# Kernel optimization log

Hardware: AMD Instinct MI355X
Metric: run time of the kernel (lower is better)

## Reference

```python
import jax, jax.numpy as jnp
import numpy as np

Q_MAX = 127.0  # 2**(8-1) - 1
EPS = 1e-08


def quantize_activation(x):
    # per-tensor symmetric int8 quant with STE
    scale = jnp.maximum(jnp.max(jnp.abs(x)) / Q_MAX, EPS)
    x_scaled = x / scale
    rounded = jnp.clip(jnp.round(x_scaled), -Q_MAX, Q_MAX)
    # STE: forward = rounded, backward = identity w.r.t. x_scaled
    q = x_scaled + jax.lax.stop_gradient(rounded - x_scaled)
    return q, jax.lax.stop_gradient(scale)


def ternarize_weight(W):
    scale = jnp.mean(jnp.abs(W)) + EPS
    W_norm = W / scale
    rounded = jnp.clip(jnp.round(W_norm), -1.0, 1.0)
    # STE: forward = rounded, backward = identity w.r.t. W
    tW = W + jax.lax.stop_gradient(rounded - W)
    return tW, jax.lax.stop_gradient(scale)


def setup_inputs() -> dict:
    key = jax.random.key(0)
    kx, kw = jax.random.split(key)
    in_features, out_features = 4096, 11008
    x = jax.random.normal(kx, (4, 2048, in_features), dtype=jnp.float32)
    # kaiming_uniform_(a=sqrt(5)) -> U(-bound, bound), bound = sqrt(6/((1+a^2)*fan_in)) = 1/sqrt(fan_in)
    bound = 1.0 / np.sqrt(in_features)
    W = jax.random.uniform(kw, (out_features, in_features), dtype=jnp.float32,
                           minval=-bound, maxval=bound)
    return {"x": x, "W": W}


def reference(x, W):
    qx, act_scale = quantize_activation(x)
    tW, w_scale = ternarize_weight(W)
    # F.linear: x @ W.T ; [b, s, in] x [out, in] -> [b, s, out]
    out = jnp.einsum('bsi,oi->bso', qx, tW)
    return out * (w_scale * act_scale)
```

## Files before the change

### kernel.cpp

```cpp
#include <hip/hip_runtime.h>
#include <cstdint>

typedef int i32x4 __attribute__((ext_vector_type(4)));
typedef int i32x16 __attribute__((ext_vector_type(16)));

#define M_DIM 8192
#define N_DIM 11008
#define K_DIM 4096
#define NT    (K_DIM / 128)

#define WS_AMAX_OFF   0
#define WS_WSUM_OFF   4096
#define WS_SCALES_OFF 12288
#define WS_QX_OFF     16384
#define WS_TW_OFF     (16384 + 33554432)

__device__ __forceinline__ void gload_lds16(const void* g, void* l) {
  __builtin_amdgcn_global_load_lds(
      (const __attribute__((address_space(1))) unsigned int*)g,
      (__attribute__((address_space(3))) unsigned int*)l, 16, 0, 0);
}


__global__ void reduce_amax(const float* __restrict__ x, float* __restrict__ partial, int n4) {
  const float4* xv = (const float4*)x;
  float m = 0.f;
  for (long i = (long)blockIdx.x * blockDim.x + threadIdx.x; i < n4;
       i += (long)gridDim.x * blockDim.x) {
    float4 v = xv[i];
    m = fmaxf(m, fmaxf(fmaxf(fabsf(v.x), fabsf(v.y)), fmaxf(fabsf(v.z), fabsf(v.w))));
  }
  __shared__ float sm[256];
  sm[threadIdx.x] = m;
  __syncthreads();
  for (int s = 128; s > 0; s >>= 1) {
    if (threadIdx.x < s) sm[threadIdx.x] = fmaxf(sm[threadIdx.x], sm[threadIdx.x + s]);
    __syncthreads();
  }
  if (threadIdx.x == 0) partial[blockIdx.x] = sm[0];
}

__global__ void reduce_wsum(const float* __restrict__ w, double* __restrict__ partial, int n4) {
  const float4* wv = (const float4*)w;
  double acc = 0.0;
  for (long i = (long)blockIdx.x * blockDim.x + threadIdx.x; i < n4;
       i += (long)gridDim.x * blockDim.x) {
    float4 v = wv[i];
    acc += (double)fabsf(v.x) + (double)fabsf(v.y) + (double)fabsf(v.z) + (double)fabsf(v.w);
  }
  __shared__ double sd[256];
  sd[threadIdx.x] = acc;
  __syncthreads();
  for (int s = 128; s > 0; s >>= 1) {
    if (threadIdx.x < s) sd[threadIdx.x] += sd[threadIdx.x + s];
    __syncthreads();
  }
  if (threadIdx.x == 0) partial[blockIdx.x] = sd[0];
}

__global__ void finalize_scales(const float* __restrict__ amax_p,
                                const double* __restrict__ wsum_p,
                                float* __restrict__ scales) {
  __shared__ float sm[1024];
  __shared__ double sd[1024];
  const int t = threadIdx.x;
  sm[t] = amax_p[t];
  sd[t] = wsum_p[t];
  __syncthreads();
  for (int s = 512; s > 0; s >>= 1) {
    if (t < s) {
      sm[t] = fmaxf(sm[t], sm[t + s]);
      sd[t] += sd[t + s];
    }
    __syncthreads();
  }
  if (t == 0) {
    float act_scale = fmaxf(sm[0] / 127.0f, 1e-8f);
    float w_scale = (float)(sd[0] / (double)((long long)N_DIM * K_DIM)) + 1e-8f;
    scales[0] = act_scale;
    scales[1] = w_scale;
    scales[2] = act_scale * w_scale;
  }
}


__device__ __forceinline__ int quant_clip(float v, float s, float lim) {
  float r = rintf(v / s);
  r = fminf(fmaxf(r, -lim), lim);
  return (int)r;
}

__global__ void quant_x(const float* __restrict__ x, const float* __restrict__ scales,
                        int8_t* __restrict__ q) {
  const float s = scales[0];
  const long i = (long)blockIdx.x * blockDim.x + threadIdx.x;
  const float4* xv = (const float4*)x + (i << 2);
  i32x4 pk;
#pragma unroll
  for (int j = 0; j < 4; ++j) {
    float4 v = xv[j];
    int b0 = quant_clip(v.x, s, 127.f);
    int b1 = quant_clip(v.y, s, 127.f);
    int b2 = quant_clip(v.z, s, 127.f);
    int b3 = quant_clip(v.w, s, 127.f);
    pk[j] = (b0 & 255) | ((b1 & 255) << 8) | ((b2 & 255) << 16) | (b3 << 24);
  }
  *((i32x4*)q + i) = pk;
}

__global__ void tern_w(const float* __restrict__ w, const float* __restrict__ scales,
                       int8_t* __restrict__ q) {
  const float s = scales[1];
  const long i = (long)blockIdx.x * blockDim.x + threadIdx.x;
  const float4* wv = (const float4*)w + (i << 2);
  i32x4 pk;
#pragma unroll
  for (int j = 0; j < 4; ++j) {
    float4 v = wv[j];
    int b0 = quant_clip(v.x, s, 1.f);
    int b1 = quant_clip(v.y, s, 1.f);
    int b2 = quant_clip(v.z, s, 1.f);
    int b3 = quant_clip(v.w, s, 1.f);
    pk[j] = (b0 & 255) | ((b1 & 255) << 8) | ((b2 & 255) << 16) | (b3 << 24);
  }
  *((i32x4*)q + i) = pk;
}


__global__ __launch_bounds__(512, 2) void gemm_i8(const int8_t* __restrict__ qx,
                                                  const int8_t* __restrict__ tw,
                                                  const float* __restrict__ scales,
                                                  float* __restrict__ out) {
  __shared__ __align__(16) int8_t lds[4][32768];

  const int tid = threadIdx.x;
  const int l = tid & 63;
  const int w = tid >> 6;

  const int bid = blockIdx.x;
  const int xcd = bid & 7;
  const int local = bid >> 3;
  const int ni = local >> 2;
  const int mi = (xcd << 2) + (local & 3);
  const long row0 = (long)mi << 8;
  const long col0 = (long)ni << 8;

  const int srow = tid >> 3;
  const int sch = (tid & 7) ^ (srow & 7);
  const int8_t* pA = qx + (row0 + srow) * (long)K_DIM + (sch << 4);
  const int8_t* pB = tw + (col0 + srow) * (long)K_DIM + (sch << 4);
  const int ldst = w << 10;

  auto stage_part = [&](int8_t* dA, int8_t* dB, int kt, int part) {
    const long cb = (long)kt << 7;
    gload_lds16(pA + cb + ((long)part * 64) * K_DIM, dA + part * 8192 + ldst);
    gload_lds16(pB + cb + ((long)part * 64) * K_DIM, dB + part * 8192 + ldst);
  };

  const int lane31 = l & 31;
  const int khalf = l >> 5;
  const int swz = l & 7;
  int cOff[4];
#pragma unroll
  for (int ks = 0; ks < 4; ++ks) cOff[ks] = ((((ks << 1) | khalf) ^ swz) << 4);
  const int aRow = ((w >> 2) * 128 + lane31) * 128;
  const int bRow0 = ((w & 3) * 64 + lane31) * 128;
  const int bRow1 = bRow0 + 32 * 128;

  i32x16 acc[4][2];
#pragma unroll
  for (int mf = 0; mf < 4; ++mf)
#pragma unroll
    for (int nf = 0; nf < 2; ++nf)
#pragma unroll
      for (int e = 0; e < 16; ++e) acc[mf][nf][e] = 0;

#pragma unroll
  for (int p = 0; p < 4; ++p) stage_part(lds[0], lds[2], 0, p);
  stage_part(lds[1], lds[3], 1, 0);
  asm volatile("s_waitcnt vmcnt(2)" ::: "memory");
  __builtin_amdgcn_s_barrier();

  for (int t = 0; t < NT; ++t) {
    int8_t* cA = lds[t & 1];
    int8_t* cB = lds[2 + (t & 1)];
    int8_t* nA = lds[(t & 1) ^ 1];
    int8_t* nB = lds[2 + ((t & 1) ^ 1)];
    const bool pf = (t + 1 < NT);

#pragma unroll
    for (int ks = 0; ks < 4; ++ks) {
      i32x4 af[4], b0, b1;
#pragma unroll
      for (int mf = 0; mf < 4; ++mf)
        af[mf] = *(const i32x4*)(cA + aRow + mf * 4096 + cOff[ks]);
      b0 = *(const i32x4*)(cB + bRow0 + cOff[ks]);
      b1 = *(const i32x4*)(cB + bRow1 + cOff[ks]);
      if (ks < 3 && pf) stage_part(nA, nB, t + 1, ks + 1);
      asm volatile("" ::: "memory");
      __builtin_amdgcn_s_barrier();
      asm volatile("s_waitcnt lgkmcnt(0)" ::: "memory");
      __builtin_amdgcn_s_setprio(1);
#pragma unroll
      for (int mf = 0; mf < 4; ++mf) {
        acc[mf][0] = __builtin_amdgcn_mfma_i32_32x32x32_i8(af[mf], b0, acc[mf][0], 0, 0, 0);
        acc[mf][1] = __builtin_amdgcn_mfma_i32_32x32x32_i8(af[mf], b1, acc[mf][1], 0, 0, 0);
      }
      __builtin_amdgcn_s_setprio(0);
      asm volatile("" ::: "memory");
      __builtin_amdgcn_s_barrier();
    }

    if (pf) {
      if (t + 2 < NT) {
        stage_part(cA, cB, t + 2, 0);
        asm volatile("s_waitcnt vmcnt(2)" ::: "memory");
      } else {
        asm volatile("s_waitcnt vmcnt(0)" ::: "memory");
      }
      __builtin_amdgcn_s_barrier();
    }
  }

  const float osc = scales[2];
  const int rbase = khalf << 2;
#pragma unroll
  for (int mf = 0; mf < 4; ++mf)
#pragma unroll
    for (int nf = 0; nf < 2; ++nf)
#pragma unroll
      for (int reg = 0; reg < 16; ++reg) {
        int rr = (w >> 2) * 128 + mf * 32 + rbase + (reg & 3) + ((reg >> 2) << 3);
        int cc = (w & 3) * 64 + nf * 32 + lane31;
        out[(row0 + rr) * (long)N_DIM + (col0 + cc)] = (float)acc[mf][nf][reg] * osc;
      }
}


extern "C" void kernel_launch(void* const* d_in, const int* in_sizes, int n_in,
                              void* d_out, int out_size, void* d_ws, size_t ws_size,
                              hipStream_t stream) {
  const float* x = (const float*)d_in[0];
  const float* W = (const float*)d_in[1];
  float* out = (float*)d_out;

  char* ws = (char*)d_ws;
  float*  amax_p = (float*)(ws + WS_AMAX_OFF);
  double* wsum_p = (double*)(ws + WS_WSUM_OFF);
  float*  scales = (float*)(ws + WS_SCALES_OFF);
  int8_t* qx = (int8_t*)(ws + WS_QX_OFF);
  int8_t* tw = (int8_t*)(ws + WS_TW_OFF);

  reduce_amax<<<1024, 256, 0, stream>>>(x, amax_p, (M_DIM * (long)K_DIM) / 4);
  reduce_wsum<<<1024, 256, 0, stream>>>(W, wsum_p, (N_DIM * (long)K_DIM) / 4);
  finalize_scales<<<1, 1024, 0, stream>>>(amax_p, wsum_p, scales);
  quant_x<<<(M_DIM * (long)K_DIM) / 16 / 256, 256, 0, stream>>>(x, scales, qx);
  tern_w<<<(N_DIM * (long)K_DIM) / 16 / 256, 256, 0, stream>>>(W, scales, tw);

  const int grid = (M_DIM / 256) * (N_DIM / 256);
  gemm_i8<<<grid, 512, 0, stream>>>(qx, tw, scales, out);
}
```

Before: 541.7 us.

## Restructure int8 GEMM main loop into 4-deep 64-wide K pipeline

Replaces the double-buffered 128-wide K tiles with four LDS stages of 64-wide K tiles and a new row-interleaved, XOR-swizzled LDS layout. Each iteration waits on vmcnt, issues one prefetch three tiles ahead, and uses a single barrier instead of several barriers per sub-step. The goal is to hide global-to-LDS latency better and cut synchronisation overhead. The trade-off is one barrier per 16 MFMAs, and the last iterations issue redundant loads of the final tile to keep the wait counts uniform.

```diff
diff --git a/kernel.cpp b/kernel.cpp
--- a/kernel.cpp
+++ b/kernel.cpp
@@ -7,7 +7,8 @@
 #define M_DIM 8192
 #define N_DIM 11008
 #define K_DIM 4096
-#define NT    (K_DIM / 128)
+#define NTILES 64
+#define DEPTH 4
 
 #define WS_AMAX_OFF   0
 #define WS_WSUM_OFF   4096
@@ -131,11 +132,13 @@
                                                   const int8_t* __restrict__ tw,
                                                   const float* __restrict__ scales,
                                                   float* __restrict__ out) {
-  __shared__ __align__(16) int8_t lds[4][32768];
+  __shared__ __align__(16) int8_t lds[DEPTH][32768];
 
   const int tid = threadIdx.x;
   const int l = tid & 63;
   const int w = tid >> 6;
+  const int lane31 = l & 31;
+  const int khalf = l >> 5;
 
   const int bid = blockIdx.x;
   const int xcd = bid & 7;
@@ -145,27 +148,28 @@
   const long row0 = (long)mi << 8;
   const long col0 = (long)ni << 8;
 
-  const int srow = tid >> 3;
-  const int sch = (tid & 7) ^ (srow & 7);
-  const int8_t* pA = qx + (row0 + srow) * (long)K_DIM + (sch << 4);
-  const int8_t* pB = tw + (col0 + srow) * (long)K_DIM + (sch << 4);
-  const int ldst = w << 10;
-
-  auto stage_part = [&](int8_t* dA, int8_t* dB, int kt, int part) {
-    const long cb = (long)kt << 7;
-    gload_lds16(pA + cb + ((long)part * 64) * K_DIM, dA + part * 8192 + ldst);
-    gload_lds16(pB + cb + ((long)part * 64) * K_DIM, dB + part * 8192 + ldst);
+  const int srow = ((l >> 3) << 1) + ((l >> 2) & 1);
+  const int schk = ((l & 3) ^ ((l >> 3) & 3)) << 4;
+  const int8_t* pA = qx + (row0 + 32 * w + srow) * (long)K_DIM + schk;
+  const int8_t* pB = tw + (col0 + 32 * w + srow) * (long)K_DIM + schk;
+  const int ldsA = w << 11;
+  const int ldsB = 16384 + (w << 11);
+
+  auto stage = [&](int d, int kt) {
+    const long cb = (long)kt << 6;
+    gload_lds16(pA + cb, lds[d] + ldsA);
+    gload_lds16(pA + cb + 16 * (long)K_DIM, lds[d] + ldsA + 1024);
+    gload_lds16(pB + cb, lds[d] + ldsB);
+    gload_lds16(pB + cb + 16 * (long)K_DIM, lds[d] + ldsB + 1024);
   };
 
-  const int lane31 = l & 31;
-  const int khalf = l >> 5;
-  const int swz = l & 7;
-  int cOff[4];
-#pragma unroll
-  for (int ks = 0; ks < 4; ++ks) cOff[ks] = ((((ks << 1) | khalf) ^ swz) << 4);
-  const int aRow = ((w >> 2) * 128 + lane31) * 128;
-  const int bRow0 = ((w & 3) * 64 + lane31) * 128;
-  const int bRow1 = bRow0 + 32 * 128;
+  const int rbl = ((lane31 >> 1) << 7) + ((lane31 & 1) << 6);
+  const int x4 = (lane31 >> 1) & 3;
+  int cOffR[4];
+#pragma unroll
+  for (int c = 0; c < 4; ++c) cOffR[c] = ((c ^ x4) << 4);
+  const int aBase = ((w >> 2) << 13) + rbl;
+  const int bBase = 16384 + ((w & 3) << 12) + rbl;
 
   i32x16 acc[4][2];
 #pragma unroll
@@ -175,51 +179,46 @@
 #pragma unroll
       for (int e = 0; e < 16; ++e) acc[mf][nf][e] = 0;
 
-#pragma unroll
-  for (int p = 0; p < 4; ++p) stage_part(lds[0], lds[2], 0, p);
-  stage_part(lds[1], lds[3], 1, 0);
-  asm volatile("s_waitcnt vmcnt(2)" ::: "memory");
-  __builtin_amdgcn_s_barrier();
-
-  for (int t = 0; t < NT; ++t) {
-    int8_t* cA = lds[t & 1];
-    int8_t* cB = lds[2 + (t & 1)];
-    int8_t* nA = lds[(t & 1) ^ 1];
-    int8_t* nB = lds[2 + ((t & 1) ^ 1)];
-    const bool pf = (t + 1 < NT);
-
-#pragma unroll
-    for (int ks = 0; ks < 4; ++ks) {
-      i32x4 af[4], b0, b1;
-#pragma unroll
-      for (int mf = 0; mf < 4; ++mf)
-        af[mf] = *(const i32x4*)(cA + aRow + mf * 4096 + cOff[ks]);
-      b0 = *(const i32x4*)(cB + bRow0 + cOff[ks]);
-      b1 = *(const i32x4*)(cB + bRow1 + cOff[ks]);
-      if (ks < 3 && pf) stage_part(nA, nB, t + 1, ks + 1);
-      asm volatile("" ::: "memory");
-      __builtin_amdgcn_s_barrier();
-      asm volatile("s_waitcnt lgkmcnt(0)" ::: "memory");
-      __builtin_amdgcn_s_setprio(1);
-#pragma unroll
-      for (int mf = 0; mf < 4; ++mf) {
-        acc[mf][0] = __builtin_amdgcn_mfma_i32_32x32x32_i8(af[mf], b0, acc[mf][0], 0, 0, 0);
-        acc[mf][1] = __builtin_amdgcn_mfma_i32_32x32x32_i8(af[mf], b1, acc[mf][1], 0, 0, 0);
-      }
-      __builtin_amdgcn_s_setprio(0);
-      asm volatile("" ::: "memory");
-      __builtin_amdgcn_s_barrier();
-    }
-
-    if (pf) {
-      if (t + 2 < NT) {
-        stage_part(cA, cB, t + 2, 0);
-        asm volatile("s_waitcnt vmcnt(2)" ::: "memory");
-      } else {
-        asm volatile("s_waitcnt vmcnt(0)" ::: "memory");
-      }
-      __builtin_amdgcn_s_barrier();
-    }
+  stage(0, 0);
+  stage(1, 1);
+  stage(2, 2);
+
+#pragma unroll 4
+  for (int t = 0; t < NTILES; ++t) {
+    asm volatile("s_waitcnt vmcnt(8)" ::: "memory");
+    asm volatile("s_waitcnt lgkmcnt(0)" ::: "memory");
+    __builtin_amdgcn_s_barrier();
+    asm volatile("" ::: "memory");
+
+    const int kt3 = (t + 3 < NTILES) ? t + 3 : NTILES - 1;
+    stage((t + 3) & 3, kt3);
+
+    const int8_t* buf = lds[t & 3];
+
+    i32x4 a0[4], a1[4], b0[2], b1[2];
+#pragma unroll
+    for (int mf = 0; mf < 4; ++mf) {
+      a0[mf] = *(const i32x4*)(buf + aBase + mf * 2048 + cOffR[khalf]);
+      a1[mf] = *(const i32x4*)(buf + aBase + mf * 2048 + cOffR[2 + khalf]);
+    }
+#pragma unroll
+    for (int nf = 0; nf < 2; ++nf) {
+      b0[nf] = *(const i32x4*)(buf + bBase + nf * 2048 + cOffR[khalf]);
+      b1[nf] = *(const i32x4*)(buf + bBase + nf * 2048 + cOffR[2 + khalf]);
+    }
+
+    __builtin_amdgcn_s_setprio(1);
+#pragma unroll
+    for (int mf = 0; mf < 4; ++mf) {
+      acc[mf][0] = __builtin_amdgcn_mfma_i32_32x32x32_i8(a0[mf], b0[0], acc[mf][0], 0, 0, 0);
+      acc[mf][1] = __builtin_amdgcn_mfma_i32_32x32x32_i8(a0[mf], b0[1], acc[mf][1], 0, 0, 0);
+    }
+#pragma unroll
+    for (int mf = 0; mf < 4; ++mf) {
+      acc[mf][0] = __builtin_amdgcn_mfma_i32_32x32x32_i8(a1[mf], b1[0], acc[mf][0], 0, 0, 0);
+      acc[mf][1] = __builtin_amdgcn_mfma_i32_32x32x32_i8(a1[mf], b1[1], acc[mf][1], 0, 0, 0);
+    }
+    __builtin_amdgcn_s_setprio(0);
   }
 
   const float osc = scales[2];
```

After: 552.2 us. About the same (+1.9%).
